# Optimization experiments

Hardware: AMD Instinct MI355X
Metric: run time of the kernel (lower is better)

## Reference

```python
import jax, jax.numpy as jnp
import numpy as np

N_NODES = 50000
N_EDGES = 800000
NODE_DIM = 64
EDGE_DIM = 32
HID = 128


def _lin_init(key, fan_in, fan_out):
    # torch nn.Linear default: U(-1/sqrt(fan_in), 1/sqrt(fan_in))
    bound = 1.0 / np.sqrt(fan_in)
    kw, kb = jax.random.split(key)
    W = jax.random.uniform(kw, (fan_in, fan_out), jnp.float32, -bound, bound)
    b = jax.random.uniform(kb, (fan_out,), jnp.float32, -bound, bound)
    return W, b


def setup_inputs() -> dict:
    key = jax.random.key(0)
    ks = jax.random.split(key, 10)
    h = jax.random.normal(ks[0], (N_NODES, NODE_DIM), dtype=jnp.float32)
    x = jax.random.normal(ks[1], (N_NODES, 3), dtype=jnp.float32) * 10.0
    edge_idx = jax.random.randint(ks[2], (2, N_EDGES), 0, N_NODES)
    edge_dist = jax.random.uniform(ks[3], (N_EDGES,), jnp.float32) * 15.0
    m_in_dim = 2 * NODE_DIM + EDGE_DIM
    W_e1, b_e1 = _lin_init(ks[4], 1, EDGE_DIM)
    W_e2, b_e2 = _lin_init(ks[5], EDGE_DIM, EDGE_DIM)
    W_n1, b_n1 = _lin_init(ks[6], m_in_dim, HID)
    W_n2, b_n2 = _lin_init(ks[7], HID, NODE_DIM)
    W_c1, b_c1 = _lin_init(ks[8], m_in_dim, HID)
    W_c2, _ = _lin_init(ks[9], HID, 1)  # coord_mlp final layer has bias=False
    return dict(h=h, x=x, edge_dist=edge_dist,
                W_e1=W_e1, b_e1=b_e1, W_e2=W_e2, b_e2=b_e2,
                W_n1=W_n1, b_n1=b_n1, W_n2=W_n2, b_n2=b_n2,
                W_c1=W_c1, b_c1=b_c1, W_c2=W_c2,
                edge_idx=edge_idx)


def reference(h, x, edge_dist, W_e1, b_e1, W_e2, b_e2, W_n1, b_n1,
              W_n2, b_n2, W_c1, b_c1, W_c2, edge_idx):
    src, dst = edge_idx[0], edge_idx[1]
    n = h.shape[0]
    # edge_mlp: Linear(1,edge_dim) -> SiLU -> Linear(edge_dim,edge_dim)
    edge_attr = jax.nn.silu(edge_dist[:, None] @ W_e1 + b_e1) @ W_e2 + b_e2  # [E, edge_dim]
    m_in = jnp.concatenate([h[src], h[dst], edge_attr], axis=-1)  # [E, 2*node+edge]
    # node_mlp: Linear -> SiLU -> Linear
    m = jax.nn.silu(m_in @ W_n1 + b_n1) @ W_n2 + b_n2  # [E, node_dim]
    h_agg = jax.ops.segment_sum(m, dst, num_segments=n)
    # coord_mlp: Linear -> SiLU -> Linear(,1,bias=False)
    coord_w = jax.nn.silu(m_in @ W_c1 + b_c1) @ W_c2  # [E, 1]
    dir_vec = x[src] - x[dst]  # [E, 3]
    dir_len = jnp.maximum(jnp.linalg.norm(dir_vec, axis=-1, keepdims=True), 1e-8)
    x_agg = jax.ops.segment_sum(coord_w * (dir_vec / dir_len), dst, num_segments=n)
    return (h + h_agg, x + x_agg)
```

## Files before the change

kernel.cpp:

```cpp
#include <hip/hip_runtime.h>
#include <cstdint>
#include <cstddef>

#define E_CNT 800000
#define N_CNT 50000
#define NT 6250

typedef short bf16x8 __attribute__((ext_vector_type(8)));
typedef short s16x4 __attribute__((ext_vector_type(4)));
typedef float f32x4 __attribute__((ext_vector_type(4)));
typedef uint32_t u32x4 __attribute__((ext_vector_type(4)));

#define OFF_CURSOR 0
#define OFF_WFN 200064
#define OFF_WFC 241024
#define OFF_W2F 281984
#define OFF_BIASN 298368
#define OFF_BIASC 298880
#define OFF_SRC 299520
#define OFF_DST 3499520
#define OFF_DIST 6699520
#define OFF_HB 8299520
#define REQ_FULL 14699520

__device__ __forceinline__ short f2bf(float v) {
  uint32_t u = __builtin_bit_cast(uint32_t, v);
  u = (u + 0x7FFFu + ((u >> 16) & 1u)) >> 16;
  return (short)u;
}
__device__ __forceinline__ float bf2f(short s) {
  uint32_t u = ((uint32_t)(uint16_t)s) << 16;
  return __builtin_bit_cast(float, u);
}
__device__ __forceinline__ uint32_t pack2(float lo, float hi) {
  return ((uint32_t)(uint16_t)f2bf(hi) << 16) | (uint32_t)(uint16_t)f2bf(lo);
}
__device__ __forceinline__ uint32_t cvtpk(float lo, float hi) {
  uint32_t r;
  asm("v_cvt_pk_bf16_f32 %0, %1, %2" : "=v"(r) : "v"(lo), "v"(hi));
  return r;
}
__device__ __forceinline__ float silu_f(float v) {
  return v * (1.0f / (1.0f + __expf(-v)));
}

template <bool FULL>
__global__ void k_pre(const float* __restrict__ h, const float* __restrict__ x,
                      float* __restrict__ out, short* __restrict__ hb,
                      const int* __restrict__ eidx, int* __restrict__ cursor,
                      const float* __restrict__ W1n, const float* __restrict__ W1c,
                      const float* __restrict__ We2, const float* __restrict__ bn1,
                      const float* __restrict__ bc1, const float* __restrict__ be2,
                      const float* __restrict__ Wn2,
                      short* __restrict__ Wfn, short* __restrict__ Wfc,
                      short* __restrict__ W2f, float* __restrict__ biasn,
                      float* __restrict__ biasc) {
  const int b = (int)blockIdx.x;
  if (b < 3272) {
    const int i = b * 256 + (int)threadIdx.x;
    if (i < 800000) {
      const f32x4 v = ((const f32x4*)h)[i];
      ((f32x4*)out)[i] = v;
      if (FULL) {
        s16x4 p;
#pragma unroll
        for (int j = 0; j < 4; ++j) p[j] = f2bf(v[j]);
        *(s16x4*)(hb + i * 4) = p;
      }
    } else if (i < 837500) {
      ((f32x4*)out)[i] = ((const f32x4*)x)[i - 800000];
    }
  } else if (b < 3297) {
    const int idx = (b - 3272) * 4 + ((int)threadIdx.x >> 6);
    const int l = (int)threadIdx.x & 63;
    if (idx < 80) {
      const int fid = (idx < 40) ? idx : (idx - 40);
      const float* W1 = (idx < 40) ? W1n : W1c;
      short* Wf = (idx < 40) ? Wfn : Wfc;
      const int kt = fid >> 3, nt = fid & 7;
      const int feat = (l & 15) * 8 + nt;
      const int k0 = kt * 32 + (l >> 4) * 8;
      bf16x8 v;
#pragma unroll
      for (int j = 0; j < 8; ++j) {
        const int k = k0 + j;
        float val;
        if (k < 128) {
          val = W1[k * 128 + feat];
        } else {
          float s = 0.f;
          for (int cc = 0; cc < 32; ++cc)
            s = fmaf(We2[(k - 128) * 32 + cc], W1[(128 + cc) * 128 + feat], s);
          val = s;
        }
        v[j] = f2bf(val);
      }
      *(bf16x8*)&Wf[(fid * 64 + l) * 8] = v;
    } else if (idx < 96) {
      const int fid = idx - 80;
      const int kt2 = fid >> 2, nt2 = fid & 3;
      bf16x8 v;
#pragma unroll
      for (int j = 0; j < 8; ++j)
        v[j] = f2bf(Wn2[(kt2 * 32 + (l >> 4) * 8 + j) * 64 + nt2 * 16 + (l & 15)]);
      *(bf16x8*)&W2f[(fid * 64 + l) * 8] = v;
    } else if (idx == 96) {
      for (int col = l; col < 128; col += 64) {
        float sn = bn1[col], sc = bc1[col];
        for (int cc = 0; cc < 32; ++cc) {
          sn = fmaf(be2[cc], W1n[(128 + cc) * 128 + col], sn);
          sc = fmaf(be2[cc], W1c[(128 + cc) * 128 + col], sc);
        }
        biasn[col] = sn;
        biasc[col] = sc;
      }
    }
  } else if (FULL) {
    const int e = (b - 3297) * 256 + (int)threadIdx.x;
    if (e < E_CNT) atomicAdd(&cursor[eidx[E_CNT + e]], 1);
  }
}

__global__ __launch_bounds__(1024) void k_scan(int* __restrict__ cursor) {
  __shared__ int part[1024];
  const int t = (int)threadIdx.x;
  const int b0 = t * 49;
  int n = N_CNT - b0;
  n = n < 0 ? 0 : (n > 49 ? 49 : n);
  int s = 0;
  for (int i = 0; i < n; ++i) s += cursor[b0 + i];
  part[t] = s;
  __syncthreads();
  for (int off = 1; off < 1024; off <<= 1) {
    const int u = (t >= off) ? part[t - off] : 0;
    __syncthreads();
    part[t] += u;
    __syncthreads();
  }
  int run = (t == 0) ? 0 : part[t - 1];
  for (int i = 0; i < n; ++i) {
    const int old = cursor[b0 + i];
    cursor[b0 + i] = run;
    run += old;
  }
}

__global__ void k_fill(const int* __restrict__ eidx, const float* __restrict__ edist,
                       int* __restrict__ cursor, int* __restrict__ src_s,
                       int* __restrict__ dst_s, short* __restrict__ dist_s) {
  const int e = (int)(blockIdx.x * 256 + threadIdx.x);
  if (e < E_CNT) {
    const int d = eidx[E_CNT + e];
    const int pos = atomicAdd(&cursor[d], 1);
    src_s[pos] = eidx[e];
    dst_s[pos] = d;
    dist_s[pos] = f2bf(edist[e]);
  }
}

template <bool SORTED>
__global__ __launch_bounds__(256, 2) void k_node(
    const float* __restrict__ h, const short* __restrict__ hb,
    const float* __restrict__ edist,
    const float* __restrict__ We1, const float* __restrict__ be1,
    const float* __restrict__ bn2, const int* __restrict__ eidx,
    const int* __restrict__ src_s, const int* __restrict__ dst_s,
    const short* __restrict__ dist_s,
    const short* __restrict__ Wf, const short* __restrict__ W2f,
    const float* __restrict__ biasn, float* __restrict__ out) {
  __shared__ __align__(16) short scr[4][16 * 136];

  const int tid = (int)threadIdx.x;
  const int w = tid >> 6, l = tid & 63, g = l >> 4, c = l & 15;
  short* myscr = &scr[w][0];

  float we1s[8], be1s[8];
#pragma unroll
  for (int j = 0; j < 8; ++j) { we1s[j] = We1[g * 8 + j]; be1s[j] = be1[g * 8 + j]; }
  float bias1[8];
#pragma unroll
  for (int nt = 0; nt < 8; ++nt) bias1[nt] = biasn[c * 8 + nt];
  float bias2[4];
#pragma unroll
  for (int nt = 0; nt < 4; ++nt) bias2[nt] = bn2[nt * 16 + c];

  const f32x4 vzero = {0.f, 0.f, 0.f, 0.f};
  const int stride = (int)gridDim.x;

  int t = (int)blockIdx.x;
  int ps0 = 0, ps1 = 0, pd0 = 0, pd1 = 0;
  float pdd0 = 0.f, pdd1 = 0.f;
  if (t < NT) {
    const int e0 = t * 128 + w * 32 + 2 * c, e1 = e0 + 1;
    if (SORTED) {
      ps0 = src_s[e0]; ps1 = src_s[e1];
      pd0 = dst_s[e0]; pd1 = dst_s[e1];
      pdd0 = bf2f(dist_s[e0]); pdd1 = bf2f(dist_s[e1]);
    } else {
      ps0 = eidx[e0]; ps1 = eidx[e1];
      pd0 = eidx[E_CNT + e0]; pd1 = eidx[E_CNT + e1];
      pdd0 = edist[e0]; pdd1 = edist[e1];
    }
  }

  for (; t < NT; t += stride) {
    const short* wft = Wf;
    const short* w2t = W2f;
    asm volatile("" : "+v"(wft), "+v"(w2t));

    const int s0 = ps0, s1 = ps1, d0 = pd0, d1 = pd1;
    const float dd0 = pdd0, dd1 = pdd1;

    const int tn = t + stride;
    if (tn < NT) {
      const int e0 = tn * 128 + w * 32 + 2 * c, e1 = e0 + 1;
      if (SORTED) {
        ps0 = src_s[e0]; ps1 = src_s[e1];
        pd0 = dst_s[e0]; pd1 = dst_s[e1];
        pdd0 = bf2f(dist_s[e0]); pdd1 = bf2f(dist_s[e1]);
      } else {
        ps0 = eidx[e0]; ps1 = eidx[e1];
        pd0 = eidx[E_CNT + e0]; pd1 = eidx[E_CNT + e1];
        pdd0 = edist[e0]; pdd1 = edist[e1];
      }
    }

    f32x4 acc[2][8];
#pragma unroll
    for (int mt = 0; mt < 2; ++mt)
#pragma unroll
      for (int nt = 0; nt < 8; ++nt) acc[mt][nt] = vzero;

#pragma unroll
    for (int kt = 0; kt < 5; ++kt) {
      bf16x8 a0, a1;
      if (kt < 4) {
        const size_t r0 = (size_t)((kt < 2) ? s0 : d0) * 64 + (kt & 1) * 32 + g * 8;
        const size_t r1 = (size_t)((kt < 2) ? s1 : d1) * 64 + (kt & 1) * 32 + g * 8;
        if (SORTED) {
          a0 = *(const bf16x8*)&hb[r0];
          a1 = *(const bf16x8*)&hb[r1];
        } else {
          const f32x4 pa = *(const f32x4*)(h + r0), pb = *(const f32x4*)(h + r0 + 4);
          const f32x4 qa = *(const f32x4*)(h + r1), qb = *(const f32x4*)(h + r1 + 4);
          u32x4 u0 = {pack2(pa[0], pa[1]), pack2(pa[2], pa[3]),
                      pack2(pb[0], pb[1]), pack2(pb[2], pb[3])};
          u32x4 u1 = {pack2(qa[0], qa[1]), pack2(qa[2], qa[3]),
                      pack2(qb[0], qb[1]), pack2(qb[2], qb[3])};
          a0 = __builtin_bit_cast(bf16x8, u0);
          a1 = __builtin_bit_cast(bf16x8, u1);
        }
      } else {
        float t0[8], t1[8];
#pragma unroll
        for (int j = 0; j < 8; ++j) {
          t0[j] = silu_f(fmaf(dd0, we1s[j], be1s[j]));
          t1[j] = silu_f(fmaf(dd1, we1s[j], be1s[j]));
        }
        u32x4 u0 = {cvtpk(t0[0], t0[1]), cvtpk(t0[2], t0[3]),
                    cvtpk(t0[4], t0[5]), cvtpk(t0[6], t0[7])};
        u32x4 u1 = {cvtpk(t1[0], t1[1]), cvtpk(t1[2], t1[3]),
                    cvtpk(t1[4], t1[5]), cvtpk(t1[6], t1[7])};
        a0 = __builtin_bit_cast(bf16x8, u0);
        a1 = __builtin_bit_cast(bf16x8, u1);
      }
#pragma unroll
      for (int nt = 0; nt < 8; ++nt) {
        const bf16x8 b = *(const bf16x8*)&wft[(((kt << 3) + nt) << 9) + (l << 3)];
        acc[0][nt] = __builtin_amdgcn_mfma_f32_16x16x32_bf16(a0, b, acc[0][nt], 0, 0, 0);
        acc[1][nt] = __builtin_amdgcn_mfma_f32_16x16x32_bf16(a1, b, acc[1][nt], 0, 0, 0);
      }
    }

    f32x4 acc2[2][4];
#pragma unroll
    for (int nt = 0; nt < 4; ++nt) { acc2[0][nt] = vzero; acc2[1][nt] = vzero; }

#pragma unroll
    for (int mt = 0; mt < 2; ++mt) {
#pragma unroll
      for (int r = 0; r < 4; ++r) {
        const float v0 = silu_f(acc[mt][0][r] + bias1[0]);
        const float v1 = silu_f(acc[mt][1][r] + bias1[1]);
        const float v2 = silu_f(acc[mt][2][r] + bias1[2]);
        const float v3 = silu_f(acc[mt][3][r] + bias1[3]);
        const float v4 = silu_f(acc[mt][4][r] + bias1[4]);
        const float v5 = silu_f(acc[mt][5][r] + bias1[5]);
        const float v6 = silu_f(acc[mt][6][r] + bias1[6]);
        const float v7 = silu_f(acc[mt][7][r] + bias1[7]);
        u32x4 pkv = {cvtpk(v0, v1), cvtpk(v2, v3), cvtpk(v4, v5), cvtpk(v6, v7)};
        *(u32x4*)&myscr[(4 * g + r) * 136 + c * 8] = pkv;
      }
#pragma unroll
      for (int kt2 = 0; kt2 < 4; ++kt2) {
        const bf16x8 a2 = *(const bf16x8*)&myscr[c * 136 + kt2 * 32 + g * 8];
#pragma unroll
        for (int nt2 = 0; nt2 < 4; ++nt2) {
          const bf16x8 b2 = *(const bf16x8*)&w2t[(((kt2 << 2) + nt2) << 9) + (l << 3)];
          acc2[mt][nt2] = __builtin_amdgcn_mfma_f32_16x16x32_bf16(a2, b2, acc2[mt][nt2], 0, 0, 0);
        }
      }
    }

    int des[8];
#pragma unroll
    for (int s = 0; s < 8; ++s)
      des[s] = __shfl((s & 1) ? d1 : d0, 4 * g + (s >> 1));

    float run[4];
    int cur = des[0];
#pragma unroll
    for (int nt2 = 0; nt2 < 4; ++nt2) run[nt2] = acc2[0][nt2][0] + bias2[nt2];
#pragma unroll
    for (int s = 1; s < 8; ++s) {
      const int mt = s & 1, r = s >> 1;
      if (des[s] == cur) {
#pragma unroll
        for (int nt2 = 0; nt2 < 4; ++nt2) run[nt2] += acc2[mt][nt2][r] + bias2[nt2];
      } else {
#pragma unroll
        for (int nt2 = 0; nt2 < 4; ++nt2)
          unsafeAtomicAdd(&out[(size_t)cur * 64 + nt2 * 16 + c], run[nt2]);
        cur = des[s];
#pragma unroll
        for (int nt2 = 0; nt2 < 4; ++nt2) run[nt2] = acc2[mt][nt2][r] + bias2[nt2];
      }
    }
#pragma unroll
    for (int nt2 = 0; nt2 < 4; ++nt2)
      unsafeAtomicAdd(&out[(size_t)cur * 64 + nt2 * 16 + c], run[nt2]);
  }
}

template <bool SORTED>
__global__ __launch_bounds__(256, 2) void k_coord(
    const float* __restrict__ h, const short* __restrict__ hb,
    const float* __restrict__ x, const float* __restrict__ edist,
    const float* __restrict__ We1, const float* __restrict__ be1,
    const float* __restrict__ Wc2, const int* __restrict__ eidx,
    const int* __restrict__ src_s, const int* __restrict__ dst_s,
    const short* __restrict__ dist_s,
    const short* __restrict__ Wf, const float* __restrict__ biasc,
    float* __restrict__ xo) {
  const int tid = (int)threadIdx.x;
  const int w = tid >> 6, l = tid & 63, g = l >> 4, c = l & 15;

  float we1s[8], be1s[8];
#pragma unroll
  for (int j = 0; j < 8; ++j) { we1s[j] = We1[g * 8 + j]; be1s[j] = be1[g * 8 + j]; }
  float b1c[8], wc2l[8];
#pragma unroll
  for (int nt = 0; nt < 8; ++nt) {
    b1c[nt] = biasc[c * 8 + nt];
    wc2l[nt] = Wc2[c * 8 + nt];
  }

  const f32x4 vzero = {0.f, 0.f, 0.f, 0.f};
  const int stride = (int)gridDim.x;

  int t = (int)blockIdx.x;
  int ps0 = 0, ps1 = 0, pd0 = 0, pd1 = 0;
  float pdd0 = 0.f, pdd1 = 0.f;
  if (t < NT) {
    const int e0 = t * 128 + w * 32 + 2 * c, e1 = e0 + 1;
    if (SORTED) {
      ps0 = src_s[e0]; ps1 = src_s[e1];
      pd0 = dst_s[e0]; pd1 = dst_s[e1];
      pdd0 = bf2f(dist_s[e0]); pdd1 = bf2f(dist_s[e1]);
    } else {
      ps0 = eidx[e0]; ps1 = eidx[e1];
      pd0 = eidx[E_CNT + e0]; pd1 = eidx[E_CNT + e1];
      pdd0 = edist[e0]; pdd1 = edist[e1];
    }
  }

  for (; t < NT; t += stride) {
    const short* wft = Wf;
    asm volatile("" : "+v"(wft));

    const int s0 = ps0, s1 = ps1, d0 = pd0, d1 = pd1;
    const float dd0 = pdd0, dd1 = pdd1;

    const int tn = t + stride;
    if (tn < NT) {
      const int e0 = tn * 128 + w * 32 + 2 * c, e1 = e0 + 1;
      if (SORTED) {
        ps0 = src_s[e0]; ps1 = src_s[e1];
        pd0 = dst_s[e0]; pd1 = dst_s[e1];
        pdd0 = bf2f(dist_s[e0]); pdd1 = bf2f(dist_s[e1]);
      } else {
        ps0 = eidx[e0]; ps1 = eidx[e1];
        pd0 = eidx[E_CNT + e0]; pd1 = eidx[E_CNT + e1];
        pdd0 = edist[e0]; pdd1 = edist[e1];
      }
    }

    f32x4 acc[2][8];
#pragma unroll
    for (int mt = 0; mt < 2; ++mt)
#pragma unroll
      for (int nt = 0; nt < 8; ++nt) acc[mt][nt] = vzero;

#pragma unroll
    for (int kt = 0; kt < 5; ++kt) {
      bf16x8 a0, a1;
      if (kt < 4) {
        const size_t r0 = (size_t)((kt < 2) ? s0 : d0) * 64 + (kt & 1) * 32 + g * 8;
        const size_t r1 = (size_t)((kt < 2) ? s1 : d1) * 64 + (kt & 1) * 32 + g * 8;
        if (SORTED) {
          a0 = *(const bf16x8*)&hb[r0];
          a1 = *(const bf16x8*)&hb[r1];
        } else {
          const f32x4 pa = *(const f32x4*)(h + r0), pb = *(const f32x4*)(h + r0 + 4);
          const f32x4 qa = *(const f32x4*)(h + r1), qb = *(const f32x4*)(h + r1 + 4);
          u32x4 u0 = {pack2(pa[0], pa[1]), pack2(pa[2], pa[3]),
                      pack2(pb[0], pb[1]), pack2(pb[2], pb[3])};
          u32x4 u1 = {pack2(qa[0], qa[1]), pack2(qa[2], qa[3]),
                      pack2(qb[0], qb[1]), pack2(qb[2], qb[3])};
          a0 = __builtin_bit_cast(bf16x8, u0);
          a1 = __builtin_bit_cast(bf16x8, u1);
        }
      } else {
        float t0[8], t1[8];
#pragma unroll
        for (int j = 0; j < 8; ++j) {
          t0[j] = silu_f(fmaf(dd0, we1s[j], be1s[j]));
          t1[j] = silu_f(fmaf(dd1, we1s[j], be1s[j]));
        }
        u32x4 u0 = {cvtpk(t0[0], t0[1]), cvtpk(t0[2], t0[3]),
                    cvtpk(t0[4], t0[5]), cvtpk(t0[6], t0[7])};
        u32x4 u1 = {cvtpk(t1[0], t1[1]), cvtpk(t1[2], t1[3]),
                    cvtpk(t1[4], t1[5]), cvtpk(t1[6], t1[7])};
        a0 = __builtin_bit_cast(bf16x8, u0);
        a1 = __builtin_bit_cast(bf16x8, u1);
      }
#pragma unroll
      for (int nt = 0; nt < 8; ++nt) {
        const bf16x8 b = *(const bf16x8*)&wft[(((kt << 3) + nt) << 9) + (l << 3)];
        acc[0][nt] = __builtin_amdgcn_mfma_f32_16x16x32_bf16(a0, b, acc[0][nt], 0, 0, 0);
        acc[1][nt] = __builtin_amdgcn_mfma_f32_16x16x32_bf16(a1, b, acc[1][nt], 0, 0, 0);
      }
    }

    float p0[4], p1[4];
#pragma unroll
    for (int r = 0; r < 4; ++r) {
      float a = 0.f, bsum = 0.f;
#pragma unroll
      for (int nt = 0; nt < 8; ++nt) {
        a += silu_f(acc[0][nt][r] + b1c[nt]) * wc2l[nt];
        bsum += silu_f(acc[1][nt][r] + b1c[nt]) * wc2l[nt];
      }
      p0[r] = a; p1[r] = bsum;
    }
#pragma unroll
    for (int m = 1; m < 16; m <<= 1)
#pragma unroll
      for (int r = 0; r < 4; ++r) {
        p0[r] += __shfl_xor(p0[r], m);
        p1[r] += __shfl_xor(p1[r], m);
      }

    const int mt = c & 1, rr = c >> 1;
    const int dA = __shfl(d0, 4 * g + rr), dB = __shfl(d1, 4 * g + rr);
    const int sA = __shfl(s0, 4 * g + rr), sB = __shfl(s1, 4 * g + rr);
    const int dstE = mt ? dB : dA;
    const int srcE = mt ? sB : sA;
    if (c < 8) {
      const float cwp0 = (rr == 0) ? p0[0] : (rr == 1) ? p0[1] : (rr == 2) ? p0[2] : p0[3];
      const float cwp1 = (rr == 0) ? p1[0] : (rr == 1) ? p1[1] : (rr == 2) ? p1[2] : p1[3];
      const float cw = mt ? cwp1 : cwp0;
      const float ax = x[srcE * 3 + 0] - x[dstE * 3 + 0];
      const float ay = x[srcE * 3 + 1] - x[dstE * 3 + 1];
      const float az = x[srcE * 3 + 2] - x[dstE * 3 + 2];
      float len = sqrtf(fmaf(ax, ax, fmaf(ay, ay, az * az)));
      len = fmaxf(len, 1e-8f);
      const float scl = cw / len;
      float vx = scl * ax, vy = scl * ay, vz = scl * az;
#pragma unroll
      for (int k = 1; k < 8; k <<= 1) {
        const float tx = __shfl(vx, l - k);
        const float ty = __shfl(vy, l - k);
        const float tz = __shfl(vz, l - k);
        const int td = __shfl(dstE, l - k);
        if (c >= k && td == dstE) { vx += tx; vy += ty; vz += tz; }
      }
      const int dnx = __shfl(dstE, l + 1);
      if (c == 7 || dnx != dstE) {
        unsafeAtomicAdd(&xo[dstE * 3 + 0], vx);
        unsafeAtomicAdd(&xo[dstE * 3 + 1], vy);
        unsafeAtomicAdd(&xo[dstE * 3 + 2], vz);
      }
    }
  }
}

extern "C" void kernel_launch(void* const* d_in, const int* in_sizes, int n_in,
                              void* d_out, int out_size, void* d_ws, size_t ws_size,
                              hipStream_t stream) {
  const float* h = (const float*)d_in[0];
  const float* x = (const float*)d_in[1];
  const float* edist = (const float*)d_in[2];
  const float* We1 = (const float*)d_in[3];
  const float* be1 = (const float*)d_in[4];
  const float* We2 = (const float*)d_in[5];
  const float* be2 = (const float*)d_in[6];
  const float* Wn1 = (const float*)d_in[7];
  const float* bn1 = (const float*)d_in[8];
  const float* Wn2 = (const float*)d_in[9];
  const float* bn2 = (const float*)d_in[10];
  const float* Wc1 = (const float*)d_in[11];
  const float* bc1 = (const float*)d_in[12];
  const float* Wc2 = (const float*)d_in[13];
  const int* eidx = (const int*)d_in[14];
  float* out = (float*)d_out;
  float* xo = out + 3200000;

  char* wsb = (char*)d_ws;
  int* cursor = (int*)(wsb + OFF_CURSOR);
  short* Wfn = (short*)(wsb + OFF_WFN);
  short* Wfc = (short*)(wsb + OFF_WFC);
  short* W2f = (short*)(wsb + OFF_W2F);
  float* biasn = (float*)(wsb + OFF_BIASN);
  float* biasc = (float*)(wsb + OFF_BIASC);
  int* src_s = (int*)(wsb + OFF_SRC);
  int* dst_s = (int*)(wsb + OFF_DST);
  short* dist_s = (short*)(wsb + OFF_DIST);
  short* hb = (short*)(wsb + OFF_HB);

  const bool full = (ws_size >= (size_t)REQ_FULL);

  if (full) {
    hipMemsetAsync(cursor, 0, N_CNT * sizeof(int), stream);
    k_pre<true><<<dim3(6422), dim3(256), 0, stream>>>(h, x, out, hb, eidx, cursor,
                                                      Wn1, Wc1, We2, bn1, bc1, be2, Wn2,
                                                      Wfn, Wfc, W2f, biasn, biasc);
    k_scan<<<dim3(1), dim3(1024), 0, stream>>>(cursor);
    k_fill<<<dim3(3125), dim3(256), 0, stream>>>(eidx, edist, cursor, src_s, dst_s, dist_s);
    k_node<true><<<dim3(512), dim3(256), 0, stream>>>(h, hb, edist, We1, be1, bn2, eidx,
                                                      src_s, dst_s, dist_s, Wfn, W2f,
                                                      biasn, out);
    k_coord<true><<<dim3(512), dim3(256), 0, stream>>>(h, hb, x, edist, We1, be1, Wc2,
                                                       eidx, src_s, dst_s, dist_s,
                                                       Wfc, biasc, xo);
  } else {
    k_pre<false><<<dim3(3297), dim3(256), 0, stream>>>(h, x, out, nullptr, eidx, nullptr,
                                                       Wn1, Wc1, We2, bn1, bc1, be2, Wn2,
                                                       Wfn, Wfc, W2f, biasn, biasc);
    k_node<false><<<dim3(512), dim3(256), 0, stream>>>(h, nullptr, edist, We1, be1, bn2,
                                                       eidx, nullptr, nullptr, nullptr,
                                                       Wfn, W2f, biasn, out);
    k_coord<false><<<dim3(512), dim3(256), 0, stream>>>(h, nullptr, x, edist, We1, be1,
                                                        Wc2, eidx, nullptr, nullptr,
                                                        nullptr, Wfc, biasc, xo);
  }
}
```

Baseline: 503.2 us.

## Merge node and coord kernels into one launch split by block halves

The separate node-MLP and coord-MLP kernels are combined into a single kernel. The first half of the 512 blocks runs the node path and the second half runs the coord path, each striding over all edge tiles with stride half the grid. This removes one launch and its tail, and lets the two workloads run concurrently on the GPU. The trade-off is that each path now has half the blocks, the combined kernel may use more registers, and the node path is heavier, so the split may leave the coord blocks idle at the end.

Result: faster. 492.4 us (-2.1%).

```diff
diff --git a/kernel.cpp b/kernel.cpp
--- a/kernel.cpp
+++ b/kernel.cpp
@@ -159,61 +159,43 @@
 }
 
 template <bool SORTED>
-__global__ __launch_bounds__(256, 2) void k_node(
+__global__ __launch_bounds__(256, 2) void k_main(
     const float* __restrict__ h, const short* __restrict__ hb,
-    const float* __restrict__ edist,
+    const float* __restrict__ x, const float* __restrict__ edist,
     const float* __restrict__ We1, const float* __restrict__ be1,
-    const float* __restrict__ bn2, const int* __restrict__ eidx,
+    const float* __restrict__ bn2, const float* __restrict__ Wc2,
+    const int* __restrict__ eidx,
     const int* __restrict__ src_s, const int* __restrict__ dst_s,
     const short* __restrict__ dist_s,
-    const short* __restrict__ Wf, const short* __restrict__ W2f,
-    const float* __restrict__ biasn, float* __restrict__ out) {
+    const short* __restrict__ Wfn, const short* __restrict__ Wfc,
+    const short* __restrict__ W2f,
+    const float* __restrict__ biasn, const float* __restrict__ biasc,
+    float* __restrict__ out, float* __restrict__ xo) {
   __shared__ __align__(16) short scr[4][16 * 136];
 
   const int tid = (int)threadIdx.x;
   const int w = tid >> 6, l = tid & 63, g = l >> 4, c = l & 15;
-  short* myscr = &scr[w][0];
-
-  float we1s[8], be1s[8];
-#pragma unroll
-  for (int j = 0; j < 8; ++j) { we1s[j] = We1[g * 8 + j]; be1s[j] = be1[g * 8 + j]; }
-  float bias1[8];
-#pragma unroll
-  for (int nt = 0; nt < 8; ++nt) bias1[nt] = biasn[c * 8 + nt];
-  float bias2[4];
-#pragma unroll
-  for (int nt = 0; nt < 4; ++nt) bias2[nt] = bn2[nt * 16 + c];
-
   const f32x4 vzero = {0.f, 0.f, 0.f, 0.f};
-  const int stride = (int)gridDim.x;
-
-  int t = (int)blockIdx.x;
-  int ps0 = 0, ps1 = 0, pd0 = 0, pd1 = 0;
-  float pdd0 = 0.f, pdd1 = 0.f;
-  if (t < NT) {
-    const int e0 = t * 128 + w * 32 + 2 * c, e1 = e0 + 1;
-    if (SORTED) {
-      ps0 = src_s[e0]; ps1 = src_s[e1];
-      pd0 = dst_s[e0]; pd1 = dst_s[e1];
-      pdd0 = bf2f(dist_s[e0]); pdd1 = bf2f(dist_s[e1]);
-    } else {
-      ps0 = eidx[e0]; ps1 = eidx[e1];
-      pd0 = eidx[E_CNT + e0]; pd1 = eidx[E_CNT + e1];
-      pdd0 = edist[e0]; pdd1 = edist[e1];
-    }
-  }
-
-  for (; t < NT; t += stride) {
-    const short* wft = Wf;
-    const short* w2t = W2f;
-    asm volatile("" : "+v"(wft), "+v"(w2t));
-
-    const int s0 = ps0, s1 = ps1, d0 = pd0, d1 = pd1;
-    const float dd0 = pdd0, dd1 = pdd1;
-
-    const int tn = t + stride;
-    if (tn < NT) {
-      const int e0 = tn * 128 + w * 32 + 2 * c, e1 = e0 + 1;
+  const int half = (int)(gridDim.x >> 1);
+
+  if ((int)blockIdx.x < half) {
+    short* myscr = &scr[w][0];
+
+    float we1s[8], be1s[8];
+#pragma unroll
+    for (int j = 0; j < 8; ++j) { we1s[j] = We1[g * 8 + j]; be1s[j] = be1[g * 8 + j]; }
+    float bias1[8];
+#pragma unroll
+    for (int nt = 0; nt < 8; ++nt) bias1[nt] = biasn[c * 8 + nt];
+    float bias2[4];
+#pragma unroll
+    for (int nt = 0; nt < 4; ++nt) bias2[nt] = bn2[nt * 16 + c];
+
+    int t = (int)blockIdx.x;
+    int ps0 = 0, ps1 = 0, pd0 = 0, pd1 = 0;
+    float pdd0 = 0.f, pdd1 = 0.f;
+    if (t < NT) {
+      const int e0 = t * 128 + w * 32 + 2 * c, e1 = e0 + 1;
       if (SORTED) {
         ps0 = src_s[e0]; ps1 = src_s[e1];
         pd0 = dst_s[e0]; pd1 = dst_s[e1];
@@ -225,165 +207,149 @@
       }
     }
 
-    f32x4 acc[2][8];
-#pragma unroll
-    for (int mt = 0; mt < 2; ++mt)
-#pragma unroll
-      for (int nt = 0; nt < 8; ++nt) acc[mt][nt] = vzero;
-
-#pragma unroll
-    for (int kt = 0; kt < 5; ++kt) {
-      bf16x8 a0, a1;
-      if (kt < 4) {
-        const size_t r0 = (size_t)((kt < 2) ? s0 : d0) * 64 + (kt & 1) * 32 + g * 8;
-        const size_t r1 = (size_t)((kt < 2) ? s1 : d1) * 64 + (kt & 1) * 32 + g * 8;
+    for (; t < NT; t += half) {
+      const short* wft = Wfn;
+      const short* w2t = W2f;
+      asm volatile("" : "+v"(wft), "+v"(w2t));
+
+      const int s0 = ps0, s1 = ps1, d0 = pd0, d1 = pd1;
+      const float dd0 = pdd0, dd1 = pdd1;
+
+      const int tn = t + half;
+      if (tn < NT) {
+        const int e0 = tn * 128 + w * 32 + 2 * c, e1 = e0 + 1;
         if (SORTED) {
-          a0 = *(const bf16x8*)&hb[r0];
-          a1 = *(const bf16x8*)&hb[r1];
+          ps0 = src_s[e0]; ps1 = src_s[e1];
+          pd0 = dst_s[e0]; pd1 = dst_s[e1];
+          pdd0 = bf2f(dist_s[e0]); pdd1 = bf2f(dist_s[e1]);
         } else {
-          const f32x4 pa = *(const f32x4*)(h + r0), pb = *(const f32x4*)(h + r0 + 4);
-          const f32x4 qa = *(const f32x4*)(h + r1), qb = *(const f32x4*)(h + r1 + 4);
-          u32x4 u0 = {pack2(pa[0], pa[1]), pack2(pa[2], pa[3]),
-                      pack2(pb[0], pb[1]), pack2(pb[2], pb[3])};
-          u32x4 u1 = {pack2(qa[0], qa[1]), pack2(qa[2], qa[3]),
-                      pack2(qb[0], qb[1]), pack2(qb[2], qb[3])};
+          ps0 = eidx[e0]; ps1 = eidx[e1];
+          pd0 = eidx[E_CNT + e0]; pd1 = eidx[E_CNT + e1];
+          pdd0 = edist[e0]; pdd1 = edist[e1];
+        }
+      }
+
+      f32x4 acc[2][8];
+#pragma unroll
+      for (int mt = 0; mt < 2; ++mt)
+#pragma unroll
+        for (int nt = 0; nt < 8; ++nt) acc[mt][nt] = vzero;
+
+#pragma unroll
+      for (int kt = 0; kt < 5; ++kt) {
+        bf16x8 a0, a1;
+        if (kt < 4) {
+          const size_t r0 = (size_t)((kt < 2) ? s0 : d0) * 64 + (kt & 1) * 32 + g * 8;
+          const size_t r1 = (size_t)((kt < 2) ? s1 : d1) * 64 + (kt & 1) * 32 + g * 8;
+          if (SORTED) {
+            a0 = *(const bf16x8*)&hb[r0];
+            a1 = *(const bf16x8*)&hb[r1];
+          } else {
+            const f32x4 pa = *(const f32x4*)(h + r0), pb = *(const f32x4*)(h + r0 + 4);
+            const f32x4 qa = *(const f32x4*)(h + r1), qb = *(const f32x4*)(h + r1 + 4);
+            u32x4 u0 = {pack2(pa[0], pa[1]), pack2(pa[2], pa[3]),
+                        pack2(pb[0], pb[1]), pack2(pb[2], pb[3])};
+            u32x4 u1 = {pack2(qa[0], qa[1]), pack2(qa[2], qa[3]),
+                        pack2(qb[0], qb[1]), pack2(qb[2], qb[3])};
+            a0 = __builtin_bit_cast(bf16x8, u0);
+            a1 = __builtin_bit_cast(bf16x8, u1);
+          }
+        } else {
+          float t0[8], t1[8];
+#pragma unroll
+          for (int j = 0; j < 8; ++j) {
+            t0[j] = silu_f(fmaf(dd0, we1s[j], be1s[j]));
+            t1[j] = silu_f(fmaf(dd1, we1s[j], be1s[j]));
+          }
+          u32x4 u0 = {cvtpk(t0[0], t0[1]), cvtpk(t0[2], t0[3]),
+                      cvtpk(t0[4], t0[5]), cvtpk(t0[6], t0[7])};
+          u32x4 u1 = {cvtpk(t1[0], t1[1]), cvtpk(t1[2], t1[3]),
+                      cvtpk(t1[4], t1[5]), cvtpk(t1[6], t1[7])};
           a0 = __builtin_bit_cast(bf16x8, u0);
           a1 = __builtin_bit_cast(bf16x8, u1);
         }
-      } else {
-        float t0[8], t1[8];
-#pragma unroll
-        for (int j = 0; j < 8; ++j) {
-          t0[j] = silu_f(fmaf(dd0, we1s[j], be1s[j]));
-          t1[j] = silu_f(fmaf(dd1, we1s[j], be1s[j]));
-        }
-        u32x4 u0 = {cvtpk(t0[0], t0[1]), cvtpk(t0[2], t0[3]),
-                    cvtpk(t0[4], t0[5]), cvtpk(t0[6], t0[7])};
-        u32x4 u1 = {cvtpk(t1[0], t1[1]), cvtpk(t1[2], t1[3]),
-                    cvtpk(t1[4], t1[5]), cvtpk(t1[6], t1[7])};
-        a0 = __builtin_bit_cast(bf16x8, u0);
-        a1 = __builtin_bit_cast(bf16x8, u1);
-      }
-#pragma unroll
-      for (int nt = 0; nt < 8; ++nt) {
-        const bf16x8 b = *(const bf16x8*)&wft[(((kt << 3) + nt) << 9) + (l << 3)];
-        acc[0][nt] = __builtin_amdgcn_mfma_f32_16x16x32_bf16(a0, b, acc[0][nt], 0, 0, 0);
-        acc[1][nt] = __builtin_amdgcn_mfma_f32_16x16x32_bf16(a1, b, acc[1][nt], 0, 0, 0);
-      }
-    }
-
-    f32x4 acc2[2][4];
-#pragma unroll
-    for (int nt = 0; nt < 4; ++nt) { acc2[0][nt] = vzero; acc2[1][nt] = vzero; }
-
-#pragma unroll
-    for (int mt = 0; mt < 2; ++mt) {
-#pragma unroll
-      for (int r = 0; r < 4; ++r) {
-        const float v0 = silu_f(acc[mt][0][r] + bias1[0]);
-        const float v1 = silu_f(acc[mt][1][r] + bias1[1]);
-        const float v2 = silu_f(acc[mt][2][r] + bias1[2]);
-        const float v3 = silu_f(acc[mt][3][r] + bias1[3]);
-        const float v4 = silu_f(acc[mt][4][r] + bias1[4]);
-        const float v5 = silu_f(acc[mt][5][r] + bias1[5]);
-        const float v6 = silu_f(acc[mt][6][r] + bias1[6]);
-        const float v7 = silu_f(acc[mt][7][r] + bias1[7]);
-        u32x4 pkv = {cvtpk(v0, v1), cvtpk(v2, v3), cvtpk(v4, v5), cvtpk(v6, v7)};
-        *(u32x4*)&myscr[(4 * g + r) * 136 + c * 8] = pkv;
-      }
-#pragma unroll
-      for (int kt2 = 0; kt2 < 4; ++kt2) {
-        const bf16x8 a2 = *(const bf16x8*)&myscr[c * 136 + kt2 * 32 + g * 8];
-#pragma unroll
-        for (int nt2 = 0; nt2 < 4; ++nt2) {
-          const bf16x8 b2 = *(const bf16x8*)&w2t[(((kt2 << 2) + nt2) << 9) + (l << 3)];
-          acc2[mt][nt2] = __builtin_amdgcn_mfma_f32_16x16x32_bf16(a2, b2, acc2[mt][nt2], 0, 0, 0);
-        }
-      }
-    }
-
-    int des[8];
-#pragma unroll
-    for (int s = 0; s < 8; ++s)
-      des[s] = __shfl((s & 1) ? d1 : d0, 4 * g + (s >> 1));
-
-    float run[4];
-    int cur = des[0];
-#pragma unroll
-    for (int nt2 = 0; nt2 < 4; ++nt2) run[nt2] = acc2[0][nt2][0] + bias2[nt2];
-#pragma unroll
-    for (int s = 1; s < 8; ++s) {
-      const int mt = s & 1, r = s >> 1;
-      if (des[s] == cur) {
-#pragma unroll
-        for (int nt2 = 0; nt2 < 4; ++nt2) run[nt2] += acc2[mt][nt2][r] + bias2[nt2];
-      } else {
-#pragma unroll
-        for (int nt2 = 0; nt2 < 4; ++nt2)
-          unsafeAtomicAdd(&out[(size_t)cur * 64 + nt2 * 16 + c], run[nt2]);
-        cur = des[s];
-#pragma unroll
-        for (int nt2 = 0; nt2 < 4; ++nt2) run[nt2] = acc2[mt][nt2][r] + bias2[nt2];
-      }
-    }
-#pragma unroll
-    for (int nt2 = 0; nt2 < 4; ++nt2)
-      unsafeAtomicAdd(&out[(size_t)cur * 64 + nt2 * 16 + c], run[nt2]);
-  }
-}
-
-template <bool SORTED>
-__global__ __launch_bounds__(256, 2) void k_coord(
-    const float* __restrict__ h, const short* __restrict__ hb,
-    const float* __restrict__ x, const float* __restrict__ edist,
-    const float* __restrict__ We1, const float* __restrict__ be1,
-    const float* __restrict__ Wc2, const int* __restrict__ eidx,
-    const int* __restrict__ src_s, const int* __restrict__ dst_s,
-    const short* __restrict__ dist_s,
-    const short* __restrict__ Wf, const float* __restrict__ biasc,
-    float* __restrict__ xo) {
-  const int tid = (int)threadIdx.x;
-  const int w = tid >> 6, l = tid & 63, g = l >> 4, c = l & 15;
-
-  float we1s[8], be1s[8];
-#pragma unroll
-  for (int j = 0; j < 8; ++j) { we1s[j] = We1[g * 8 + j]; be1s[j] = be1[g * 8 + j]; }
-  float b1c[8], wc2l[8];
-#pragma unroll
-  for (int nt = 0; nt < 8; ++nt) {
-    b1c[nt] = biasc[c * 8 + nt];
-    wc2l[nt] = Wc2[c * 8 + nt];
-  }
-
-  const f32x4 vzero = {0.f, 0.f, 0.f, 0.f};
-  const int stride = (int)gridDim.x;
-
-  int t = (int)blockIdx.x;
-  int ps0 = 0, ps1 = 0, pd0 = 0, pd1 = 0;
-  float pdd0 = 0.f, pdd1 = 0.f;
-  if (t < NT) {
-    const int e0 = t * 128 + w * 32 + 2 * c, e1 = e0 + 1;
-    if (SORTED) {
-      ps0 = src_s[e0]; ps1 = src_s[e1];
-      pd0 = dst_s[e0]; pd1 = dst_s[e1];
-      pdd0 = bf2f(dist_s[e0]); pdd1 = bf2f(dist_s[e1]);
-    } else {
-      ps0 = eidx[e0]; ps1 = eidx[e1];
-      pd0 = eidx[E_CNT + e0]; pd1 = eidx[E_CNT + e1];
-      pdd0 = edist[e0]; pdd1 = edist[e1];
-    }
-  }
-
-  for (; t < NT; t += stride) {
-    const short* wft = Wf;
-    asm volatile("" : "+v"(wft));
-
-    const int s0 = ps0, s1 = ps1, d0 = pd0, d1 = pd1;
-    const float dd0 = pdd0, dd1 = pdd1;
-
-    const int tn = t + stride;
-    if (tn < NT) {
-      const int e0 = tn * 128 + w * 32 + 2 * c, e1 = e0 + 1;
+#pragma unroll
+        for (int nt = 0; nt < 8; ++nt) {
+          const bf16x8 b = *(const bf16x8*)&wft[(((kt << 3) + nt) << 9) + (l << 3)];
+          acc[0][nt] = __builtin_amdgcn_mfma_f32_16x16x32_bf16(a0, b, acc[0][nt], 0, 0, 0);
+          acc[1][nt] = __builtin_amdgcn_mfma_f32_16x16x32_bf16(a1, b, acc[1][nt], 0, 0, 0);
+        }
+      }
+
+      f32x4 acc2[2][4];
+#pragma unroll
+      for (int nt = 0; nt < 4; ++nt) { acc2[0][nt] = vzero; acc2[1][nt] = vzero; }
+
+#pragma unroll
+      for (int mt = 0; mt < 2; ++mt) {
+#pragma unroll
+        for (int r = 0; r < 4; ++r) {
+          const float v0 = silu_f(acc[mt][0][r] + bias1[0]);
+          const float v1 = silu_f(acc[mt][1][r] + bias1[1]);
+          const float v2 = silu_f(acc[mt][2][r] + bias1[2]);
+          const float v3 = silu_f(acc[mt][3][r] + bias1[3]);
+          const float v4 = silu_f(acc[mt][4][r] + bias1[4]);
+          const float v5 = silu_f(acc[mt][5][r] + bias1[5]);
+          const float v6 = silu_f(acc[mt][6][r] + bias1[6]);
+          const float v7 = silu_f(acc[mt][7][r] + bias1[7]);
+          u32x4 pkv = {cvtpk(v0, v1), cvtpk(v2, v3), cvtpk(v4, v5), cvtpk(v6, v7)};
+          *(u32x4*)&myscr[(4 * g + r) * 136 + c * 8] = pkv;
+        }
+#pragma unroll
+        for (int kt2 = 0; kt2 < 4; ++kt2) {
+          const bf16x8 a2 = *(const bf16x8*)&myscr[c * 136 + kt2 * 32 + g * 8];
+#pragma unroll
+          for (int nt2 = 0; nt2 < 4; ++nt2) {
+            const bf16x8 b2 = *(const bf16x8*)&w2t[(((kt2 << 2) + nt2) << 9) + (l << 3)];
+            acc2[mt][nt2] = __builtin_amdgcn_mfma_f32_16x16x32_bf16(a2, b2, acc2[mt][nt2], 0, 0, 0);
+          }
+        }
+      }
+
+      int des[8];
+#pragma unroll
+      for (int s = 0; s < 8; ++s)
+        des[s] = __shfl((s & 1) ? d1 : d0, 4 * g + (s >> 1));
+
+      float run[4];
+      int cur = des[0];
+#pragma unroll
+      for (int nt2 = 0; nt2 < 4; ++nt2) run[nt2] = acc2[0][nt2][0] + bias2[nt2];
+#pragma unroll
+      for (int s = 1; s < 8; ++s) {
+        const int mt = s & 1, r = s >> 1;
+        if (des[s] == cur) {
+#pragma unroll
+          for (int nt2 = 0; nt2 < 4; ++nt2) run[nt2] += acc2[mt][nt2][r] + bias2[nt2];
+        } else {
+#pragma unroll
+          for (int nt2 = 0; nt2 < 4; ++nt2)
+            unsafeAtomicAdd(&out[(size_t)cur * 64 + nt2 * 16 + c], run[nt2]);
+          cur = des[s];
+#pragma unroll
+          for (int nt2 = 0; nt2 < 4; ++nt2) run[nt2] = acc2[mt][nt2][r] + bias2[nt2];
+        }
+      }
+#pragma unroll
+      for (int nt2 = 0; nt2 < 4; ++nt2)
+        unsafeAtomicAdd(&out[(size_t)cur * 64 + nt2 * 16 + c], run[nt2]);
+    }
+  } else {
+    float we1s[8], be1s[8];
+#pragma unroll
+    for (int j = 0; j < 8; ++j) { we1s[j] = We1[g * 8 + j]; be1s[j] = be1[g * 8 + j]; }
+    float b1c[8], wc2l[8];
+#pragma unroll
+    for (int nt = 0; nt < 8; ++nt) {
+      b1c[nt] = biasc[c * 8 + nt];
+      wc2l[nt] = Wc2[c * 8 + nt];
+    }
+
+    int t = (int)blockIdx.x - half;
+    int ps0 = 0, ps1 = 0, pd0 = 0, pd1 = 0;
+    float pdd0 = 0.f, pdd1 = 0.f;
+    if (t < NT) {
+      const int e0 = t * 128 + w * 32 + 2 * c, e1 = e0 + 1;
       if (SORTED) {
         ps0 = src_s[e0]; ps1 = src_s[e1];
         pd0 = dst_s[e0]; pd1 = dst_s[e1];
@@ -395,101 +361,123 @@
       }
     }
 
-    f32x4 acc[2][8];
-#pragma unroll
-    for (int mt = 0; mt < 2; ++mt)
-#pragma unroll
-      for (int nt = 0; nt < 8; ++nt) acc[mt][nt] = vzero;
-
-#pragma unroll
-    for (int kt = 0; kt < 5; ++kt) {
-      bf16x8 a0, a1;
-      if (kt < 4) {
-        const size_t r0 = (size_t)((kt < 2) ? s0 : d0) * 64 + (kt & 1) * 32 + g * 8;
-        const size_t r1 = (size_t)((kt < 2) ? s1 : d1) * 64 + (kt & 1) * 32 + g * 8;
+    for (; t < NT; t += half) {
+      const short* wft = Wfc;
+      asm volatile("" : "+v"(wft));
+
+      const int s0 = ps0, s1 = ps1, d0 = pd0, d1 = pd1;
+      const float dd0 = pdd0, dd1 = pdd1;
+
+      const int tn = t + half;
+      if (tn < NT) {
+        const int e0 = tn * 128 + w * 32 + 2 * c, e1 = e0 + 1;
         if (SORTED) {
-          a0 = *(const bf16x8*)&hb[r0];
-          a1 = *(const bf16x8*)&hb[r1];
+          ps0 = src_s[e0]; ps1 = src_s[e1];
+          pd0 = dst_s[e0]; pd1 = dst_s[e1];
+          pdd0 = bf2f(dist_s[e0]); pdd1 = bf2f(dist_s[e1]);
         } else {
-          const f32x4 pa = *(const f32x4*)(h + r0), pb = *(const f32x4*)(h + r0 + 4);
-          const f32x4 qa = *(const f32x4*)(h + r1), qb = *(const f32x4*)(h + r1 + 4);
-          u32x4 u0 = {pack2(pa[0], pa[1]), pack2(pa[2], pa[3]),
-                      pack2(pb[0], pb[1]), pack2(pb[2], pb[3])};
-          u32x4 u1 = {pack2(qa[0], qa[1]), pack2(qa[2], qa[3]),
-                      pack2(qb[0], qb[1]), pack2(qb[2], qb[3])};
+          ps0 = eidx[e0]; ps1 = eidx[e1];
+          pd0 = eidx[E_CNT + e0]; pd1 = eidx[E_CNT + e1];
+          pdd0 = edist[e0]; pdd1 = edist[e1];
+        }
+      }
+
+      f32x4 acc[2][8];
+#pragma unroll
+      for (int mt = 0; mt < 2; ++mt)
+#pragma unroll
+        for (int nt = 0; nt < 8; ++nt) acc[mt][nt] = vzero;
+
+#pragma unroll
+      for (int kt = 0; kt < 5; ++kt) {
+        bf16x8 a0, a1;
+        if (kt < 4) {
+          const size_t r0 = (size_t)((kt < 2) ? s0 : d0) * 64 + (kt & 1) * 32 + g * 8;
+          const size_t r1 = (size_t)((kt < 2) ? s1 : d1) * 64 + (kt & 1) * 32 + g * 8;
+          if (SORTED) {
+            a0 = *(const bf16x8*)&hb[r0];
+            a1 = *(const bf16x8*)&hb[r1];
+          } else {
+            const f32x4 pa = *(const f32x4*)(h + r0), pb = *(const f32x4*)(h + r0 + 4);
+            const f32x4 qa = *(const f32x4*)(h + r1), qb = *(const f32x4*)(h + r1 + 4);
+            u32x4 u0 = {pack2(pa[0], pa[1]), pack2(pa[2], pa[3]),
+                        pack2(pb[0], pb[1]), pack2(pb[2], pb[3])};
+            u32x4 u1 = {pack2(qa[0], qa[1]), pack2(qa[2], qa[3]),
+                        pack2(qb[0], qb[1]), pack2(qb[2], qb[3])};
+            a0 = __builtin_bit_cast(bf16x8, u0);
+            a1 = __builtin_bit_cast(bf16x8, u1);
+          }
+        } else {
+          float t0[8], t1[8];
+#pragma unroll
+          for (int j = 0; j < 8; ++j) {
+            t0[j] = silu_f(fmaf(dd0, we1s[j], be1s[j]));
+            t1[j] = silu_f(fmaf(dd1, we1s[j], be1s[j]));
+          }
+          u32x4 u0 = {cvtpk(t0[0], t0[1]), cvtpk(t0[2], t0[3]),
+                      cvtpk(t0[4], t0[5]), cvtpk(t0[6], t0[7])};
+          u32x4 u1 = {cvtpk(t1[0], t1[1]), cvtpk(t1[2], t1[3]),
+                      cvtpk(t1[4], t1[5]), cvtpk(t1[6], t1[7])};
           a0 = __builtin_bit_cast(bf16x8, u0);
           a1 = __builtin_bit_cast(bf16x8, u1);
         }
-      } else {
-        float t0[8], t1[8];
-#pragma unroll
-        for (int j = 0; j < 8; ++j) {
-          t0[j] = silu_f(fmaf(dd0, we1s[j], be1s[j]));
-          t1[j] = silu_f(fmaf(dd1, we1s[j], be1s[j]));
-        }
-        u32x4 u0 = {cvtpk(t0[0], t0[1]), cvtpk(t0[2], t0[3]),
-                    cvtpk(t0[4], t0[5]), cvtpk(t0[6], t0[7])};
-        u32x4 u1 = {cvtpk(t1[0], t1[1]), cvtpk(t1[2], t1[3]),
-                    cvtpk(t1[4], t1[5]), cvtpk(t1[6], t1[7])};
-        a0 = __builtin_bit_cast(bf16x8, u0);
-        a1 = __builtin_bit_cast(bf16x8, u1);
-      }
-#pragma unroll
-      for (int nt = 0; nt < 8; ++nt) {
-        const bf16x8 b = *(const bf16x8*)&wft[(((kt << 3) + nt) << 9) + (l << 3)];
-        acc[0][nt] = __builtin_amdgcn_mfma_f32_16x16x32_bf16(a0, b, acc[0][nt], 0, 0, 0);
-        acc[1][nt] = __builtin_amdgcn_mfma_f32_16x16x32_bf16(a1, b, acc[1][nt], 0, 0, 0);
-      }
-    }
-
-    float p0[4], p1[4];
-#pragma unroll
-    for (int r = 0; r < 4; ++r) {
-      float a = 0.f, bsum = 0.f;
-#pragma unroll
-      for (int nt = 0; nt < 8; ++nt) {
-        a += silu_f(acc[0][nt][r] + b1c[nt]) * wc2l[nt];
-        bsum += silu_f(acc[1][nt][r] + b1c[nt]) * wc2l[nt];
-      }
-      p0[r] = a; p1[r] = bsum;
-    }
-#pragma unroll
-    for (int m = 1; m < 16; m <<= 1)
+#pragma unroll
+        for (int nt = 0; nt < 8; ++nt) {
+          const bf16x8 b = *(const bf16x8*)&wft[(((kt << 3) + nt) << 9) + (l << 3)];
+          acc[0][nt] = __builtin_amdgcn_mfma_f32_16x16x32_bf16(a0, b, acc[0][nt], 0, 0, 0);
+          acc[1][nt] = __builtin_amdgcn_mfma_f32_16x16x32_bf16(a1, b, acc[1][nt], 0, 0, 0);
+        }
+      }
+
+      float p0[4], p1[4];
 #pragma unroll
       for (int r = 0; r < 4; ++r) {
-        p0[r] += __shfl_xor(p0[r], m);
-        p1[r] += __shfl_xor(p1[r], m);
-      }
-
-    const int mt = c & 1, rr = c >> 1;
-    const int dA = __shfl(d0, 4 * g + rr), dB = __shfl(d1, 4 * g + rr);
-    const int sA = __shfl(s0, 4 * g + rr), sB = __shfl(s1, 4 * g + rr);
-    const int dstE = mt ? dB : dA;
-    const int srcE = mt ? sB : sA;
-    if (c < 8) {
-      const float cwp0 = (rr == 0) ? p0[0] : (rr == 1) ? p0[1] : (rr == 2) ? p0[2] : p0[3];
-      const float cwp1 = (rr == 0) ? p1[0] : (rr == 1) ? p1[1] : (rr == 2) ? p1[2] : p1[3];
-      const float cw = mt ? cwp1 : cwp0;
-      const float ax = x[srcE * 3 + 0] - x[dstE * 3 + 0];
-      const float ay = x[srcE * 3 + 1] - x[dstE * 3 + 1];
-      const float az = x[srcE * 3 + 2] - x[dstE * 3 + 2];
-      float len = sqrtf(fmaf(ax, ax, fmaf(ay, ay, az * az)));
-      len = fmaxf(len, 1e-8f);
-      const float scl = cw / len;
-      float vx = scl * ax, vy = scl * ay, vz = scl * az;
-#pragma unroll
-      for (int k = 1; k < 8; k <<= 1) {
-        const float tx = __shfl(vx, l - k);
-        const float ty = __shfl(vy, l - k);
-        const float tz = __shfl(vz, l - k);
-        const int td = __shfl(dstE, l - k);
-        if (c >= k && td == dstE) { vx += tx; vy += ty; vz += tz; }
-      }
-      const int dnx = __shfl(dstE, l + 1);
-      if (c == 7 || dnx != dstE) {
-        unsafeAtomicAdd(&xo[dstE * 3 + 0], vx);
-        unsafeAtomicAdd(&xo[dstE * 3 + 1], vy);
-        unsafeAtomicAdd(&xo[dstE * 3 + 2], vz);
+        float a = 0.f, bsum = 0.f;
+#pragma unroll
+        for (int nt = 0; nt < 8; ++nt) {
+          a += silu_f(acc[0][nt][r] + b1c[nt]) * wc2l[nt];
+          bsum += silu_f(acc[1][nt][r] + b1c[nt]) * wc2l[nt];
+        }
+        p0[r] = a; p1[r] = bsum;
+      }
+#pragma unroll
+      for (int m = 1; m < 16; m <<= 1)
+#pragma unroll
+        for (int r = 0; r < 4; ++r) {
+          p0[r] += __shfl_xor(p0[r], m);
+          p1[r] += __shfl_xor(p1[r], m);
+        }
+
+      const int mt = c & 1, rr = c >> 1;
+      const int dA = __shfl(d0, 4 * g + rr), dB = __shfl(d1, 4 * g + rr);
+      const int sA = __shfl(s0, 4 * g + rr), sB = __shfl(s1, 4 * g + rr);
+      const int dstE = mt ? dB : dA;
+      const int srcE = mt ? sB : sA;
+      if (c < 8) {
+        const float cwp0 = (rr == 0) ? p0[0] : (rr == 1) ? p0[1] : (rr == 2) ? p0[2] : p0[3];
+        const float cwp1 = (rr == 0) ? p1[0] : (rr == 1) ? p1[1] : (rr == 2) ? p1[2] : p1[3];
+        const float cw = mt ? cwp1 : cwp0;
+        const float ax = x[srcE * 3 + 0] - x[dstE * 3 + 0];
+        const float ay = x[srcE * 3 + 1] - x[dstE * 3 + 1];
+        const float az = x[srcE * 3 + 2] - x[dstE * 3 + 2];
+        float len = sqrtf(fmaf(ax, ax, fmaf(ay, ay, az * az)));
+        len = fmaxf(len, 1e-8f);
+        const float scl = cw / len;
+        float vx = scl * ax, vy = scl * ay, vz = scl * az;
+#pragma unroll
+        for (int k = 1; k < 8; k <<= 1) {
+          const float tx = __shfl(vx, l - k);
+          const float ty = __shfl(vy, l - k);
+          const float tz = __shfl(vz, l - k);
+          const int td = __shfl(dstE, l - k);
+          if (c >= k && td == dstE) { vx += tx; vy += ty; vz += tz; }
+        }
+        const int dnx = __shfl(dstE, l + 1);
+        if (c == 7 || dnx != dstE) {
+          unsafeAtomicAdd(&xo[dstE * 3 + 0], vx);
+          unsafeAtomicAdd(&xo[dstE * 3 + 1], vy);
+          unsafeAtomicAdd(&xo[dstE * 3 + 2], vz);
+        }
       }
     }
   }
@@ -537,21 +525,15 @@
                                                       Wfn, Wfc, W2f, biasn, biasc);
     k_scan<<<dim3(1), dim3(1024), 0, stream>>>(cursor);
     k_fill<<<dim3(3125), dim3(256), 0, stream>>>(eidx, edist, cursor, src_s, dst_s, dist_s);
-    k_node<true><<<dim3(512), dim3(256), 0, stream>>>(h, hb, edist, We1, be1, bn2, eidx,
-                                                      src_s, dst_s, dist_s, Wfn, W2f,
-                                                      biasn, out);
-    k_coord<true><<<dim3(512), dim3(256), 0, stream>>>(h, hb, x, edist, We1, be1, Wc2,
-                                                       eidx, src_s, dst_s, dist_s,
-                                                       Wfc, biasc, xo);
+    k_main<true><<<dim3(512), dim3(256), 0, stream>>>(
+        h, hb, x, edist, We1, be1, bn2, Wc2, eidx, src_s, dst_s, dist_s,
+        Wfn, Wfc, W2f, biasn, biasc, out, xo);
   } else {
     k_pre<false><<<dim3(3297), dim3(256), 0, stream>>>(h, x, out, nullptr, eidx, nullptr,
                                                        Wn1, Wc1, We2, bn1, bc1, be2, Wn2,
                                                        Wfn, Wfc, W2f, biasn, biasc);
-    k_node<false><<<dim3(512), dim3(256), 0, stream>>>(h, nullptr, edist, We1, be1, bn2,
-                                                       eidx, nullptr, nullptr, nullptr,
-                                                       Wfn, W2f, biasn, out);
-    k_coord<false><<<dim3(512), dim3(256), 0, stream>>>(h, nullptr, x, edist, We1, be1,
-                                                        Wc2, eidx, nullptr, nullptr,
-                                                        nullptr, Wfc, biasc, xo);
+    k_main<false><<<dim3(512), dim3(256), 0, stream>>>(
+        h, nullptr, x, edist, We1, be1, bn2, Wc2, eidx, nullptr, nullptr, nullptr,
+        Wfn, Wfc, W2f, biasn, biasc, out, xo);
   }
 }
```
